# Performance work log

Hardware: AMD Instinct MI355X
Metric: run time of the kernel (lower is better)

## Reference

```python
import jax, jax.numpy as jnp
import numpy as np

B, C, H, W = 4, 512, 64, 64
D = 512  # model_dim


def setup_inputs() -> dict:
    key = jax.random.key(0)
    ks = jax.random.split(key, 9)
    s = 0.02
    return {
        "q": jax.random.normal(ks[0], (B, C, H, W), dtype=jnp.float32),
        "Wq": jax.random.normal(ks[1], (D, C), dtype=jnp.float32) * s,
        "bq": jax.random.normal(ks[2], (D,), dtype=jnp.float32) * s,
        "Wk": jax.random.normal(ks[3], (D, C), dtype=jnp.float32) * s,
        "bk": jax.random.normal(ks[4], (D,), dtype=jnp.float32) * s,
        "Wv": jax.random.normal(ks[5], (D, C), dtype=jnp.float32) * s,
        "bv": jax.random.normal(ks[6], (D,), dtype=jnp.float32) * s,
        "Wo": jax.random.normal(ks[7], (C, D), dtype=jnp.float32) * s,
        "bo": jax.random.normal(ks[8], (C,), dtype=jnp.float32) * s,
    }


def reference(q, Wq, bq, Wk, bk, Wv, bv, Wo, bo):
    b, c, h, w = q.shape
    # 1x1 conv == per-pixel linear over channels; tokens s = h*w
    x = q.reshape(b, c, h * w)                      # (b, c, s)
    Q = jnp.einsum('bcs,dc->bsd', x, Wq) + bq       # (b, s, D)
    K = jnp.einsum('bcs,dc->bsd', x, Wk) + bk
    V = jnp.einsum('bcs,dc->bsd', x, Wv) + bv
    # ScaleAttend: scale = q.shape[-1]^-0.5 = model_dim^-0.5 (heads not split)
    scale = jnp.asarray(Q.shape[-1], Q.dtype) ** -0.5
    sim = jnp.einsum('bsd,btd->bst', Q, K) * scale  # (b, s, s)
    attn = jax.nn.softmax(sim, axis=-1)
    o = jnp.einsum('bst,btd->bsd', attn, V)         # (b, s, D)
    # to_out 1x1 conv: D -> C
    y = jnp.einsum('bsd,cd->bsc', o, Wo) + bo       # (b, s, C)
    return y.transpose(0, 2, 1).reshape(b, c, h, w)
```

## Files before the change

kernel.cpp:

```cpp
#include <hip/hip_runtime.h>
#include <hip/hip_bf16.h>

typedef __hip_bfloat16 bf16;
typedef __attribute__((ext_vector_type(8))) short short8;
typedef __attribute__((ext_vector_type(4))) float floatx4;
typedef __attribute__((ext_vector_type(4))) short shortx4;

static constexpr int BATCH = 4;
static constexpr int CH    = 512;
static constexpr int SEQ   = 4096;
static constexpr int DM    = 512;

__device__ __forceinline__ void gload16(const void* g, void* l) {
  __builtin_amdgcn_global_load_lds(
      (const __attribute__((address_space(1))) unsigned int*)g,
      (__attribute__((address_space(3))) unsigned int*)l,
      16, 0, 0);
}

__device__ __forceinline__ float hw_exp2(float x) {
  float r;
  asm("v_exp_f32 %0, %1" : "=v"(r) : "v"(x));
  return r;
}

__global__ __launch_bounds__(256) void cvt_weights(
    const float* __restrict__ w0, const float* __restrict__ w1,
    const float* __restrict__ w2, const float* __restrict__ w3,
    bf16* __restrict__ out) {
  const float* src = (blockIdx.y == 0) ? w0 : (blockIdx.y == 1) ? w1
                   : (blockIdx.y == 2) ? w2 : w3;
  int idx = blockIdx.x * 256 + threadIdx.x;
  out[(long)blockIdx.y * (DM * CH) + idx] = __float2bfloat16(src[idx]);
}

__global__ __launch_bounds__(256) void transpose_cvt(
    const float* __restrict__ x, bf16* __restrict__ xT) {
  __shared__ float tile[64][65];
  const int s0 = blockIdx.x * 64, c0 = blockIdx.y * 64;
  const float* xb = x + (long)blockIdx.z * CH * SEQ;
  bf16* xTb = xT + (long)blockIdx.z * SEQ * CH;
  const int t = threadIdx.x;
  const int sl = t & 63, cq = t >> 6;
  #pragma unroll
  for (int i = 0; i < 16; ++i) {
    int cl = cq * 16 + i;
    tile[cl][sl] = xb[(long)(c0 + cl) * SEQ + s0 + sl];
  }
  __syncthreads();
  const int cl2 = t & 63, sq = t >> 6;
  #pragma unroll
  for (int i = 0; i < 16; ++i) {
    int sl2 = sq * 16 + i;
    xTb[(long)(s0 + sl2) * CH + c0 + cl2] = __float2bfloat16(tile[cl2][sl2]);
  }
}

template <int KIND>
__global__ __launch_bounds__(256, 2) void proj128(
    const bf16* __restrict__ A0, const bf16* __restrict__ Wbase,
    const float* __restrict__ b0, const float* __restrict__ b1,
    const float* __restrict__ b2, void* __restrict__ Cbase) {
  __shared__ __align__(16) bf16 As[2][128 * 64];
  __shared__ __align__(16) bf16 Bs[2][128 * 64];

  int id = blockIdx.x + gridDim.x * (blockIdx.y + gridDim.y * blockIdx.z);
  int nwg = gridDim.x * gridDim.y * gridDim.z;
  int sid = ((nwg & 7) == 0) ? ((id & 7) * (nwg >> 3) + (id >> 3)) : id;
  const int bx = sid % gridDim.x;
  const int by = (sid / gridDim.x) % gridDim.y;
  const int z  = sid / (gridDim.x * gridDim.y);
  const int mat = (KIND == 0) ? (z >> 2) : 0;
  const int bz  = (KIND == 0) ? (z & 3) : z;

  const long XSZ = (long)SEQ * CH;
  const long lK = CH;
  const bf16* Ab = A0 + (long)bz * XSZ + (long)by * 128 * lK;
  const bf16* Bb = Wbase + (long)mat * ((long)DM * CH) + (long)bx * 128 * lK;
  const float* bias = (KIND == 1) ? b0 : (mat == 0 ? b0 : mat == 1 ? b1 : b2);

  const int tid = threadIdx.x;
  const int w = tid >> 6, lane = tid & 63;
  const int wr = w >> 1, wc = w & 1;
  const int l16 = lane & 15, quad = lane >> 4;
  const int srow = tid >> 3;
  const int sp = tid & 7;
  const int slog = (sp ^ (srow & 7)) << 3;
  const int pA0 = (quad ^ (l16 & 7)) << 3;
  const int pA1 = pA0 ^ 32;

  auto stageA = [&](int buf, int kt) {
    const bf16* s = Ab + kt * 64 + (long)srow * lK + slog;
    char* d = (char*)(&As[buf][0]) + tid * 16;
    #pragma unroll
    for (int r = 0; r < 4; ++r)
      gload16(s + (long)(r * 32) * lK, d + r * 4096);
  };
  auto stageB = [&](int buf, int kt) {
    const bf16* s = Bb + kt * 64 + (long)srow * lK + slog;
    char* d = (char*)(&Bs[buf][0]) + tid * 16;
    #pragma unroll
    for (int r = 0; r < 4; ++r)
      gload16(s + (long)(r * 32) * lK, d + r * 4096);
  };

  floatx4 acc[4][4];
  #pragma unroll
  for (int m = 0; m < 4; ++m)
    #pragma unroll
    for (int n = 0; n < 4; ++n) acc[m][n] = (floatx4)(0.0f);

  const int nk = CH >> 6;
  stageA(0, 0); stageB(0, 0);
  __syncthreads();

  for (int t = 0; t < nk; ++t) {
    const int cur = t & 1, nxt = cur ^ 1;
    const bool more = (t + 1 < nk);
    #pragma unroll
    for (int kc = 0; kc < 2; ++kc) {
      const int poff = kc ? pA1 : pA0;
      short8 a[4], b[4];
      #pragma unroll
      for (int i = 0; i < 4; ++i)
        a[i] = *(const short8*)(&As[cur][0] + (wr * 64 + i * 16 + l16) * 64 + poff);
      #pragma unroll
      for (int j = 0; j < 4; ++j)
        b[j] = *(const short8*)(&Bs[cur][0] + (wc * 64 + j * 16 + l16) * 64 + poff);
      if (more) {
        if (kc == 0) stageA(nxt, t + 1);
        else         stageB(nxt, t + 1);
      }
      __builtin_amdgcn_s_setprio(1);
      #pragma unroll
      for (int i = 0; i < 4; ++i)
        #pragma unroll
        for (int j = 0; j < 4; ++j)
          acc[i][j] = __builtin_amdgcn_mfma_f32_16x16x32_bf16(
              a[i], b[j], acc[i][j], 0, 0, 0);
      __builtin_amdgcn_s_setprio(0);
    }
    __syncthreads();
  }

  const int rbase = by * 128 + wr * 64 + quad * 4;
  const int cbase = bx * 128 + wc * 64 + l16;
  #pragma unroll
  for (int m = 0; m < 4; ++m) {
    const int row = rbase + m * 16;
    #pragma unroll
    for (int n = 0; n < 4; ++n) {
      const int col = cbase + n * 16;
      floatx4 v = acc[m][n];
      const float bb = bias[col];
      if constexpr (KIND == 0) {
        if (mat < 2) {
          bf16* C = (bf16*)Cbase + (long)mat * (BATCH * XSZ) + (long)bz * XSZ;
          #pragma unroll
          for (int r = 0; r < 4; ++r)
            C[(long)(row + r) * DM + col] = __float2bfloat16(v[r] + bb);
        } else {
          bf16* C = (bf16*)Cbase + 2 * (BATCH * XSZ) + (long)bz * XSZ;
          alignas(8) bf16 tmp[4];
          #pragma unroll
          for (int r = 0; r < 4; ++r) tmp[r] = __float2bfloat16(v[r] + bb);
          *(shortx4*)(C + (long)col * SEQ + row) = *(const shortx4*)tmp;
        }
      } else {
        float* C = (float*)Cbase + (long)bz * XSZ;
        floatx4 o_;
        #pragma unroll
        for (int r = 0; r < 4; ++r) o_[r] = v[r] + bb;
        *(floatx4*)(C + (long)col * SEQ + row) = o_;
      }
    }
  }
}

__global__ __launch_bounds__(512, 2) void gemm_qk(
    const bf16* __restrict__ A, long sAz,
    const bf16* __restrict__ B, long sBz,
    bf16* __restrict__ C, long sCz,
    float scale, int K, int ldc) {
  __shared__ __align__(16) bf16 As[2][256 * 64];
  __shared__ __align__(16) bf16 Bs[2][256 * 64];

  int id = blockIdx.x + gridDim.x * (blockIdx.y + gridDim.y * blockIdx.z);
  int nwg = gridDim.x * gridDim.y * gridDim.z;
  int sid = ((nwg & 7) == 0) ? ((id & 7) * (nwg >> 3) + (id >> 3)) : id;
  const int bx = sid % gridDim.x;
  const int by = (sid / gridDim.x) % gridDim.y;
  const int bz = sid / (gridDim.x * gridDim.y);

  const int tid = threadIdx.x;
  const long lK = K;
  const bf16* Ab = A + (long)bz * sAz + (long)by * 256 * lK;
  const bf16* Bb = B + (long)bz * sBz + (long)bx * 256 * lK;

  const int w = tid >> 6, lane = tid & 63;
  const int wr = w >> 2, wc = w & 3;
  const int l16 = lane & 15, quad = lane >> 4;

  const int srow = tid >> 3;
  const int sp = tid & 7;
  const int slog = (sp ^ (srow & 7)) << 3;

  const int pA0 = (quad ^ (l16 & 7)) << 3;
  const int pA1 = pA0 ^ 32;

  auto stage_half = [&](const bf16* Gb, bf16* Lb, int kt, int h) {
    #pragma unroll
    for (int r = 0; r < 2; ++r) {
      const int row = h * 128 + r * 64 + srow;
      gload16(Gb + (long)kt * 64 + (long)row * lK + slog,
              (char*)Lb + row * 128 + sp * 16);
    }
  };

  floatx4 acc[8][4];
  #pragma unroll
  for (int m = 0; m < 8; ++m)
    #pragma unroll
    for (int n = 0; n < 4; ++n) acc[m][n] = (floatx4)(0.0f);

  const int nk = K >> 6;
  stage_half(Ab, &As[0][0], 0, 0); stage_half(Bb, &Bs[0][0], 0, 0);
  stage_half(Ab, &As[0][0], 0, 1); stage_half(Bb, &Bs[0][0], 0, 1);
  if (nk > 1) { stage_half(Ab, &As[1][0], 1, 0); stage_half(Bb, &Bs[1][0], 1, 0); }
  asm volatile("s_waitcnt vmcnt(4)" ::: "memory");
  __builtin_amdgcn_s_barrier();

  for (int tt = 0; tt < nk; tt += 2) {
    #pragma unroll
    for (int u = 0; u < 2; ++u) {
      const bf16* __restrict__ Al = &As[u][0];
      const bf16* __restrict__ Bl = &Bs[u][0];
      short8 a[2][4], b[2][2][2];
      #pragma unroll
      for (int p = 0; p < 4; ++p) {
        const int rm = p >> 1, cn = p & 1;
        if (cn == 0) {
          #pragma unroll
          for (int kc = 0; kc < 2; ++kc)
            #pragma unroll
            for (int i = 0; i < 4; ++i)
              a[kc][i] = *(const short8*)(
                  Al + (rm * 128 + wr * 64 + i * 16 + l16) * 64
                     + (kc ? pA1 : pA0));
        }
        if (rm == 0) {
          #pragma unroll
          for (int kc = 0; kc < 2; ++kc)
            #pragma unroll
            for (int j = 0; j < 2; ++j)
              b[kc][cn][j] = *(const short8*)(
                  Bl + (cn * 128 + wc * 32 + j * 16 + l16) * 64
                     + (kc ? pA1 : pA0));
        }
        {
          const int g = u * 4 + p;
          const int stile = tt + 1 + ((g + 2) >> 2);
          if (stile < nk) {
            const int sh = (p < 2) ? 1 : 0;
            if (p & 1) stage_half(Bb, &Bs[stile & 1][0], stile, sh);
            else       stage_half(Ab, &As[stile & 1][0], stile, sh);
          }
        }
        __builtin_amdgcn_sched_barrier(0);
        __builtin_amdgcn_s_barrier();
        asm volatile("s_waitcnt lgkmcnt(0)" ::: "memory");
        __builtin_amdgcn_sched_barrier(0);
        __builtin_amdgcn_s_setprio(1);
        #pragma unroll
        for (int kc = 0; kc < 2; ++kc)
          #pragma unroll
          for (int i = 0; i < 4; ++i)
            #pragma unroll
            for (int j = 0; j < 2; ++j)
              acc[rm * 4 + i][cn * 2 + j] =
                  __builtin_amdgcn_mfma_f32_16x16x32_bf16(
                      a[kc][i], b[kc][cn][j], acc[rm * 4 + i][cn * 2 + j],
                      0, 0, 0);
        __builtin_amdgcn_s_setprio(0);
        if (p == 3) {
          if (u == 0) {
            if (tt + 2 < nk) asm volatile("s_waitcnt vmcnt(4)" ::: "memory");
            else             asm volatile("s_waitcnt vmcnt(0)" ::: "memory");
          } else {
            if (tt + 2 < nk) asm volatile("s_waitcnt vmcnt(4)" ::: "memory");
          }
        }
        __builtin_amdgcn_s_barrier();
      }
    }
  }

  bf16* Cb = C + (long)bz * sCz;
  #pragma unroll
  for (int rm = 0; rm < 2; ++rm)
    #pragma unroll
    for (int i = 0; i < 4; ++i) {
      const int row = by * 256 + rm * 128 + wr * 64 + i * 16 + quad * 4;
      #pragma unroll
      for (int cn = 0; cn < 2; ++cn)
        #pragma unroll
        for (int j = 0; j < 2; ++j) {
          const int col = bx * 256 + cn * 128 + wc * 32 + j * 16 + l16;
          floatx4 v = acc[rm * 4 + i][cn * 2 + j];
          #pragma unroll
          for (int r = 0; r < 4; ++r)
            Cb[(long)(row + r) * ldc + col] = __float2bfloat16(v[r] * scale);
        }
    }
}

__global__ __launch_bounds__(512, 2) void fused_smpv(
    const bf16* __restrict__ Sim, const bf16* __restrict__ Vt,
    bf16* __restrict__ Ob) {
  __shared__ __align__(16) bf16 Apv[2][64 * 64];
  __shared__ __align__(16) bf16 Bpv[2][512 * 64];
  __shared__ float rl_lds[64];

  const int id = blockIdx.x + (blockIdx.y << 6);
  const int xcd = id & 7;
  const int bz = xcd >> 1;
  const int by = ((id >> 3) << 1) | (id & 1);

  const int tid = threadIdx.x;
  const bf16* Simb = Sim + (long)bz * ((long)SEQ * SEQ) + (long)(by * 64) * SEQ;
  const bf16* Vb   = Vt  + (long)bz * ((long)SEQ * CH);
  bf16* Obb        = Ob  + (long)bz * ((long)SEQ * CH) + (long)(by * 64) * CH;

  const int srow = tid >> 3;
  const int sp = tid & 7;
  const int slog = (sp ^ (srow & 7)) << 3;
  const int aswz = (sp ^ (srow & 7)) << 4;

  const int w = tid >> 6, lane = tid & 63;
  const int l16 = lane & 15, quad = lane >> 4;
  const int pA0 = (quad ^ (l16 & 7)) << 3;
  const int pA1 = pA0 ^ 32;

  float lsum = 0.f;

  auto stageB8 = [&](int buf, int kt) {
    const bf16* s = Vb + (long)srow * SEQ + kt * 64 + slog;
    char* d = (char*)(&Bpv[buf][0]) + tid * 16;
    #pragma unroll
    for (int r = 0; r < 8; ++r)
      gload16(s + (long)(r * 64) * SEQ, d + r * 8192);
  };
  auto writeA = [&](int buf, uint4 u) {
    const ushort* h = (const ushort*)&u;
    union { uint4 u4; ushort hh[8]; } pk;
    #pragma unroll
    for (int k2 = 0; k2 < 8; ++k2) {
      float f = __uint_as_float(((unsigned)h[k2]) << 16);
      float e = hw_exp2(f);
      lsum += e;
      __hip_bfloat16 pb = __float2bfloat16(e);
      pk.hh[k2] = *(const ushort*)&pb;
    }
    *(uint4*)((char*)(&Apv[buf][0]) + srow * 128 + aswz) = pk.u4;
  };

  {
    uint4 ua = *(const uint4*)(Simb + (long)srow * SEQ + sp * 8);
    stageB8(0, 0);
    writeA(0, ua);
  }
  __syncthreads();

  floatx4 acc[4][4];
  #pragma unroll
  for (int i = 0; i < 4; ++i)
    #pragma unroll
    for (int j = 0; j < 4; ++j) acc[i][j] = (floatx4)(0.0f);

  const int nk = SEQ >> 6;
  for (int t = 0; t < nk; ++t) {
    const int cur = t & 1, nxt = cur ^ 1;
    const bool more = (t + 1 < nk);
    uint4 un;
    if (more) {
      un = *(const uint4*)(Simb + (long)srow * SEQ + (t + 1) * 64 + sp * 8);
      stageB8(nxt, t + 1);
    }
    short8 a[2][4], b[2][4];
    #pragma unroll
    for (int kc = 0; kc < 2; ++kc) {
      const int poff = kc ? pA1 : pA0;
      #pragma unroll
      for (int i = 0; i < 4; ++i)
        a[kc][i] = *(const short8*)(&Apv[cur][0] + (i * 16 + l16) * 64 + poff);
      #pragma unroll
      for (int j = 0; j < 4; ++j)
        b[kc][j] = *(const short8*)(&Bpv[cur][0]
                                    + (w * 64 + j * 16 + l16) * 64 + poff);
    }
    __builtin_amdgcn_s_setprio(1);
    #pragma unroll
    for (int kc = 0; kc < 2; ++kc)
      #pragma unroll
      for (int i = 0; i < 4; ++i)
        #pragma unroll
        for (int j = 0; j < 4; ++j)
          acc[i][j] = __builtin_amdgcn_mfma_f32_16x16x32_bf16(
              a[kc][i], b[kc][j], acc[i][j], 0, 0, 0);
    __builtin_amdgcn_s_setprio(0);
    if (more) writeA(nxt, un);
    __syncthreads();
  }

  #pragma unroll
  for (int o = 1; o < 8; o <<= 1) lsum += __shfl_xor(lsum, o);
  if (sp == 0) rl_lds[srow] = 1.0f / lsum;
  __syncthreads();

  #pragma unroll
  for (int i = 0; i < 4; ++i) {
    #pragma unroll
    for (int j = 0; j < 4; ++j) {
      floatx4 v = acc[i][j];
      const int col = w * 64 + j * 16 + l16;
      #pragma unroll
      for (int r = 0; r < 4; ++r) {
        const int row = i * 16 + quad * 4 + r;
        Obb[(long)row * CH + col] = __float2bfloat16(v[r] * rl_lds[row]);
      }
    }
  }
}

extern "C" void kernel_launch(void* const* d_in, const int* in_sizes, int n_in,
                              void* d_out, int out_size, void* d_ws,
                              size_t ws_size, hipStream_t stream) {
  const float* q  = (const float*)d_in[0];
  const float* Wq = (const float*)d_in[1];
  const float* bq = (const float*)d_in[2];
  const float* Wk = (const float*)d_in[3];
  const float* bk = (const float*)d_in[4];
  const float* Wv = (const float*)d_in[5];
  const float* bv = (const float*)d_in[6];
  const float* Wo = (const float*)d_in[7];
  const float* bo = (const float*)d_in[8];
  float* out = (float*)d_out;

  bf16* ws = (bf16*)d_ws;
  const long WSZ = (long)DM * CH;
  const long XSZ = (long)SEQ * CH;
  const long SSZ = (long)SEQ * SEQ;
  bf16* Wqb = ws;
  bf16* Wob = Wqb + 3 * WSZ;
  bf16* xT  = Wqb + 4 * WSZ;
  bf16* Qb  = xT + BATCH * XSZ;
  bf16* Kb  = Qb + BATCH * XSZ;
  bf16* Vt  = Kb + BATCH * XSZ;
  bf16* Ob  = Vt + BATCH * XSZ;
  bf16* Sim = Ob + BATCH * XSZ;

  cvt_weights<<<dim3(WSZ / 256, 4), 256, 0, stream>>>(Wq, Wk, Wv, Wo, ws);
  transpose_cvt<<<dim3(SEQ / 64, CH / 64, BATCH), 256, 0, stream>>>(q, xT);

  proj128<0><<<dim3(4, 32, 12), 256, 0, stream>>>(
      xT, Wqb, bq, bk, bv, Qb);
  const float qkscale = 0.04419417382415922f * 1.4426950408889634f;
  gemm_qk<<<dim3(16, 16, BATCH), 512, 0, stream>>>(
      Qb, XSZ, Kb, XSZ, Sim, SSZ, qkscale, CH, SEQ);
  fused_smpv<<<dim3(64, 4), 512, 0, stream>>>(Sim, Vt, Ob);
  proj128<1><<<dim3(4, 32, 4), 256, 0, stream>>>(
      Ob, Wob, bo, nullptr, nullptr, out);
}
```

Before: 342.6 us.

## Halve P*V row tile and single-buffer LDS to raise occupancy in fused_smpv

The fused exp+PV kernel now processes 32 query rows per block instead of 64 and launches twice as many blocks. Its LDS tiles are single-buffered, with a mid-iteration barrier placed after the fragment reads so the next V tile can be staged during the MFMAs. Launch bounds are raised so more blocks fit per CU. The aim is better latency hiding and better load balance across CUs, at the cost of V tiles being re-read for every 32 rows instead of every 64 and an extra barrier per iteration.

```diff
diff --git a/kernel.cpp b/kernel.cpp
--- a/kernel.cpp
+++ b/kernel.cpp
@@ -314,27 +314,31 @@
     }
 }
 
-__global__ __launch_bounds__(512, 2) void fused_smpv(
+__global__ __launch_bounds__(512, 4) void fused_smpv(
     const bf16* __restrict__ Sim, const bf16* __restrict__ Vt,
     bf16* __restrict__ Ob) {
-  __shared__ __align__(16) bf16 Apv[2][64 * 64];
-  __shared__ __align__(16) bf16 Bpv[2][512 * 64];
-  __shared__ float rl_lds[64];
-
-  const int id = blockIdx.x + (blockIdx.y << 6);
+  __shared__ __align__(16) bf16 Apv[32 * 64];
+  __shared__ __align__(16) bf16 Bpv[512 * 64];
+  __shared__ float rl_lds[32];
+
+  const int id = blockIdx.x + (blockIdx.y << 7);
   const int xcd = id & 7;
   const int bz = xcd >> 1;
   const int by = ((id >> 3) << 1) | (id & 1);
 
   const int tid = threadIdx.x;
-  const bf16* Simb = Sim + (long)bz * ((long)SEQ * SEQ) + (long)(by * 64) * SEQ;
+  const bf16* Simb = Sim + (long)bz * ((long)SEQ * SEQ) + (long)(by * 32) * SEQ;
   const bf16* Vb   = Vt  + (long)bz * ((long)SEQ * CH);
-  bf16* Obb        = Ob  + (long)bz * ((long)SEQ * CH) + (long)(by * 64) * CH;
+  bf16* Obb        = Ob  + (long)bz * ((long)SEQ * CH) + (long)(by * 32) * CH;
+
+  const int prow = tid >> 4;
+  const int pcol = (tid & 15) * 4;
+  const int pwbyte = prow * 128 + (((pcol >> 3) ^ (prow & 7)) << 4)
+                   + ((pcol & 7) << 1);
 
   const int srow = tid >> 3;
   const int sp = tid & 7;
   const int slog = (sp ^ (srow & 7)) << 3;
-  const int aswz = (sp ^ (srow & 7)) << 4;
 
   const int w = tid >> 6, lane = tid & 63;
   const int l16 = lane & 15, quad = lane >> 4;
@@ -343,82 +347,81 @@
 
   float lsum = 0.f;
 
-  auto stageB8 = [&](int buf, int kt) {
+  auto stageB8 = [&](int kt) {
     const bf16* s = Vb + (long)srow * SEQ + kt * 64 + slog;
-    char* d = (char*)(&Bpv[buf][0]) + tid * 16;
+    char* d = (char*)Bpv + tid * 16;
     #pragma unroll
     for (int r = 0; r < 8; ++r)
       gload16(s + (long)(r * 64) * SEQ, d + r * 8192);
   };
-  auto writeA = [&](int buf, uint4 u) {
+  auto loadSim = [&](int t) {
+    return *(const uint2*)(Simb + (long)prow * SEQ + t * 64 + pcol);
+  };
+  auto writeA = [&](uint2 u) {
     const ushort* h = (const ushort*)&u;
-    union { uint4 u4; ushort hh[8]; } pk;
-    #pragma unroll
-    for (int k2 = 0; k2 < 8; ++k2) {
+    union { uint2 u2; ushort hh[4]; } pk;
+    #pragma unroll
+    for (int k2 = 0; k2 < 4; ++k2) {
       float f = __uint_as_float(((unsigned)h[k2]) << 16);
       float e = hw_exp2(f);
       lsum += e;
       __hip_bfloat16 pb = __float2bfloat16(e);
       pk.hh[k2] = *(const ushort*)&pb;
     }
-    *(uint4*)((char*)(&Apv[buf][0]) + srow * 128 + aswz) = pk.u4;
-  };
-
-  {
-    uint4 ua = *(const uint4*)(Simb + (long)srow * SEQ + sp * 8);
-    stageB8(0, 0);
-    writeA(0, ua);
-  }
+    *(uint2*)((char*)Apv + pwbyte) = pk.u2;
+  };
+
+  stageB8(0);
+  writeA(loadSim(0));
   __syncthreads();
 
-  floatx4 acc[4][4];
-  #pragma unroll
-  for (int i = 0; i < 4; ++i)
+  floatx4 acc[2][4];
+  #pragma unroll
+  for (int i = 0; i < 2; ++i)
     #pragma unroll
     for (int j = 0; j < 4; ++j) acc[i][j] = (floatx4)(0.0f);
 
   const int nk = SEQ >> 6;
   for (int t = 0; t < nk; ++t) {
-    const int cur = t & 1, nxt = cur ^ 1;
     const bool more = (t + 1 < nk);
-    uint4 un;
-    if (more) {
-      un = *(const uint4*)(Simb + (long)srow * SEQ + (t + 1) * 64 + sp * 8);
-      stageB8(nxt, t + 1);
-    }
-    short8 a[2][4], b[2][4];
+    uint2 un;
+    if (more) un = loadSim(t + 1);
+    short8 a[2][2], b[2][4];
     #pragma unroll
     for (int kc = 0; kc < 2; ++kc) {
       const int poff = kc ? pA1 : pA0;
       #pragma unroll
-      for (int i = 0; i < 4; ++i)
-        a[kc][i] = *(const short8*)(&Apv[cur][0] + (i * 16 + l16) * 64 + poff);
+      for (int i = 0; i < 2; ++i)
+        a[kc][i] = *(const short8*)(Apv + (i * 16 + l16) * 64 + poff);
       #pragma unroll
       for (int j = 0; j < 4; ++j)
-        b[kc][j] = *(const short8*)(&Bpv[cur][0]
-                                    + (w * 64 + j * 16 + l16) * 64 + poff);
-    }
+        b[kc][j] = *(const short8*)(Bpv + (w * 64 + j * 16 + l16) * 64 + poff);
+    }
+    asm volatile("s_waitcnt lgkmcnt(0)" ::: "memory");
+    __builtin_amdgcn_s_barrier();
+    __builtin_amdgcn_sched_barrier(0);
+    if (more) stageB8(t + 1);
     __builtin_amdgcn_s_setprio(1);
     #pragma unroll
     for (int kc = 0; kc < 2; ++kc)
       #pragma unroll
-      for (int i = 0; i < 4; ++i)
+      for (int i = 0; i < 2; ++i)
         #pragma unroll
         for (int j = 0; j < 4; ++j)
           acc[i][j] = __builtin_amdgcn_mfma_f32_16x16x32_bf16(
               a[kc][i], b[kc][j], acc[i][j], 0, 0, 0);
     __builtin_amdgcn_s_setprio(0);
-    if (more) writeA(nxt, un);
+    if (more) writeA(un);
     __syncthreads();
   }
 
   #pragma unroll
-  for (int o = 1; o < 8; o <<= 1) lsum += __shfl_xor(lsum, o);
-  if (sp == 0) rl_lds[srow] = 1.0f / lsum;
+  for (int o = 1; o < 16; o <<= 1) lsum += __shfl_xor(lsum, o);
+  if ((tid & 15) == 0) rl_lds[prow] = 1.0f / lsum;
   __syncthreads();
 
   #pragma unroll
-  for (int i = 0; i < 4; ++i) {
+  for (int i = 0; i < 2; ++i) {
     #pragma unroll
     for (int j = 0; j < 4; ++j) {
       floatx4 v = acc[i][j];
@@ -467,7 +470,7 @@
   const float qkscale = 0.04419417382415922f * 1.4426950408889634f;
   gemm_qk<<<dim3(16, 16, BATCH), 512, 0, stream>>>(
       Qb, XSZ, Kb, XSZ, Sim, SSZ, qkscale, CH, SEQ);
-  fused_smpv<<<dim3(64, 4), 512, 0, stream>>>(Sim, Vt, Ob);
+  fused_smpv<<<dim3(128, 4), 512, 0, stream>>>(Sim, Vt, Ob);
   proj128<1><<<dim3(4, 32, 4), 256, 0, stream>>>(
       Ob, Wob, bo, nullptr, nullptr, out);
 }
```

New measurement: 344.3 us. No clear change (+0.5%).
